# Performance work log

Measured on AMD Instinct MI355X. Metric: run time of the kernel, lower is better.

Reference implementation:

```python
import jax, jax.numpy as jnp
import numpy as np

N, E, D_LM, H, L, C = 100000, 1000000, 1024, 128, 3, 8


def setup_inputs() -> dict:
    key = jax.random.key(0)
    ks = jax.random.split(key, 8)
    return {
        "last_hidden_state": jax.random.normal(ks[0], (N, D_LM), jnp.float32),
        "edge_index": jax.random.randint(ks[1], (2, E), 0, N, dtype=jnp.int32),
        "W_lm": jax.random.normal(ks[2], (D_LM, H), jnp.float32) * 0.03,
        "b_lm": jnp.zeros((H,), jnp.float32),
        "W_gcn": jax.random.normal(ks[3], (L, H, H), jnp.float32) * 0.08,
        "b_gcn": jnp.zeros((L, H), jnp.float32),
        "W_cls": jax.random.normal(ks[4], (2 * H, C), jnp.float32) * 0.06,
        "b_cls": jnp.zeros((C,), jnp.float32),
    }


def reference(last_hidden_state, edge_index, W_lm, b_lm, W_gcn, b_gcn, W_cls, b_cls):
    # Frozen LM output -> lm_head (dropout is identity in eval mode)
    n = last_hidden_state.shape[0]
    lm = last_hidden_state @ W_lm + b_lm                      # [N, H]

    # GCN normalization (add self-loops, symmetric deg^{-1/2} norm), shared by all layers
    loops = jnp.arange(n, dtype=edge_index.dtype)
    src = jnp.concatenate([edge_index[0], loops])             # message sources j
    dst = jnp.concatenate([edge_index[1], loops])             # aggregation targets i
    deg = jax.ops.segment_sum(jnp.ones_like(dst, jnp.float32), dst, num_segments=n)
    dinv = jax.lax.rsqrt(jnp.maximum(deg, 1.0))               # deg >= 1 due to self-loops
    norm = dinv[src] * dinv[dst]                              # [E+N]

    out = lm
    for l in range(W_gcn.shape[0]):
        h = out @ W_gcn[l]                                    # linear transform first (PyG GCNConv)
        msg = h[src] * norm[:, None]                          # gather + scale  [E+N, H]
        out = jax.ops.segment_sum(msg, dst, num_segments=n) + b_gcn[l]
        out = jax.nn.relu(out)                                # dropout identity in eval

    logits = jnp.concatenate([lm, out], axis=-1) @ W_cls + b_cls  # [N, C]
    return logits
```

## Files before the change

### kernel.cpp

```cpp
#include <hip/hip_runtime.h>


using bf16x8 = __attribute__((ext_vector_type(8))) short;
using f32x4  = __attribute__((ext_vector_type(4))) float;
typedef unsigned short u16;
typedef unsigned int   u32;

__device__ __forceinline__ u16 f2bf(float f) {
  u32 u = __builtin_bit_cast(u32, f);
  u += 0x7fffu + ((u >> 16) & 1u);
  return (u16)(u >> 16);
}
__device__ __forceinline__ float bf2f(u32 lo16) {
  return __builtin_bit_cast(float, lo16 << 16);
}
__device__ __forceinline__ u32 packbf2(float a, float b) {
  u32 r;
  asm("v_cvt_pk_bf16_f32 %0, %1, %2" : "=v"(r) : "v"(a), "v"(b));
  return r;
}
__device__ __forceinline__ void gl_lds16(const void* g, void* l) {
  __builtin_amdgcn_global_load_lds(
      (const __attribute__((address_space(1))) void*)g,
      (__attribute__((address_space(3))) void*)l, 16, 0, 0);
}


__global__ void prep_fat(const float* __restrict__ Wlm, u16* __restrict__ WlmT,
                         const float* __restrict__ Wg, u16* __restrict__ WgT, int totalG) {
  int b = blockIdx.x;
  if (b < 512) {
    int idx = b * 256 + threadIdx.x;
    int k = idx >> 7, c = idx & 127;
    WlmT[c * 1024 + k] = f2bf(Wlm[idx]);
  } else {
    int idx = (b - 512) * 256 + threadIdx.x;
    if (idx < totalG) {
      int l = idx >> 14; int r = idx & 16383;
      int k = r >> 7, c = r & 127;
      WgT[l * 16384 + c * 128 + k] = f2bf(Wg[idx]);
    }
  }
}


__global__ void dinv_scanpart(const int* __restrict__ counts, float* __restrict__ dinv,
                              int* __restrict__ partials, int N) {
  __shared__ int sdata[256];
  int t = threadIdx.x;
  int base = blockIdx.x * 1024 + t * 4;
  int s = 0;
#pragma unroll
  for (int i = 0; i < 4; i++) {
    int idx = base + i;
    if (idx < N) {
      int c = counts[idx];
      s += c;
      dinv[idx] = rsqrtf((float)(c + 1));
    }
  }
  sdata[t] = s; __syncthreads();
  for (int off = 128; off > 0; off >>= 1) {
    if (t < off) sdata[t] += sdata[t + off];
    __syncthreads();
  }
  if (t == 0) partials[blockIdx.x] = sdata[0];
}


__global__ void scan_final2(const int* __restrict__ counts, const int* __restrict__ partials,
                            int* __restrict__ offsets, int N, int E, int NB) {
  __shared__ int sdata[256];
  int t = threadIdx.x;
  int pv = (t < NB && t < (int)blockIdx.x) ? partials[t] : 0;
  sdata[t] = pv; __syncthreads();
  for (int off = 128; off > 0; off >>= 1) {
    if (t < off) sdata[t] += sdata[t + off];
    __syncthreads();
  }
  int bse = sdata[0];
  __syncthreads();

  int bofs = blockIdx.x * 1024 + t * 4;
  int v[4]; int tsum = 0;
#pragma unroll
  for (int i = 0; i < 4; i++) { int idx = bofs + i; v[i] = (idx < N) ? counts[idx] : 0; tsum += v[i]; }
  sdata[t] = tsum; __syncthreads();
  int val = tsum;
  for (int off = 1; off < 256; off <<= 1) {
    int add = (t >= off) ? sdata[t - off] : 0;
    __syncthreads();
    val += add; sdata[t] = val;
    __syncthreads();
  }
  int run = bse + val - tsum;
#pragma unroll
  for (int i = 0; i < 4; i++) { int idx = bofs + i; if (idx < N) offsets[idx] = run; run += v[i]; }
  if (blockIdx.x == 0 && t == 0) offsets[N] = E;
}


__global__ __launch_bounds__(256) void gemm_lm_count_kernel(
    const float* __restrict__ A, const u16* __restrict__ Bt,
    const float* __restrict__ bias, u16* __restrict__ Out, int Nrows,
    const int* __restrict__ dst, int* __restrict__ counts, int E, int GB)
{
  __shared__ u16 lA[2][128 * 32];
  __shared__ u16 lB[2][128 * 32];
  if ((int)blockIdx.x >= GB) {
    int e = ((int)blockIdx.x - GB) * 256 + threadIdx.x;
    if (e < E) atomicAdd(&counts[dst[e]], 1);
    return;
  }
  const int t = threadIdx.x;
  const int lane = t & 63;
  const int w = t >> 6;
  const int wr = w >> 1, wc = w & 1;
  const long rowbase = (long)blockIdx.x * 128;
  const int quad = lane >> 4;
  const int l16 = lane & 15;

  const int seg0 = t, seg1 = t + 256;
  const int r0 = seg0 >> 2, kq0 = seg0 & 3;
  const int r1 = seg1 >> 2, kq1 = seg1 & 3;
  long g0 = rowbase + r0; if (g0 >= Nrows) g0 = Nrows - 1;
  long g1 = rowbase + r1; if (g1 >= Nrows) g1 = Nrows - 1;
  const float* Ab0 = A + g0 * 1024 + kq0 * 8;
  const float* Ab1 = A + g1 * 1024 + kq1 * 8;
  const int dA0 = (seg0 * 16) ^ ((r0 & 3) << 4);
  const int dA1 = (seg1 * 16) ^ ((r1 & 3) << 4);
  const char* Bsrc0 = (const char*)Bt + (size_t)r0 * 2048 + ((kq0 ^ (r0 & 3)) << 4);
  const char* Bsrc1 = (const char*)Bt + (size_t)r1 * 2048 + ((kq1 ^ (r1 & 3)) << 4);
  const int dB0 = seg0 * 16, dB1 = seg1 * 16;

  f32x4 acc[4][4];
#pragma unroll
  for (int i = 0; i < 4; i++)
#pragma unroll
    for (int j = 0; j < 4; j++) acc[i][j] = f32x4{0.f, 0.f, 0.f, 0.f};

  float4 fa[2][4];

#define GLB(KS, BUF) do { \
    gl_lds16(Bsrc0 + (size_t)(KS) * 64, (char*)lB[BUF] + dB0); \
    gl_lds16(Bsrc1 + (size_t)(KS) * 64, (char*)lB[BUF] + dB1); \
  } while (0)

#define ALOAD(KS, S) do { \
    fa[S][0] = *reinterpret_cast<const float4*>(Ab0 + (KS) * 32); \
    fa[S][1] = *reinterpret_cast<const float4*>(Ab0 + (KS) * 32 + 4); \
    fa[S][2] = *reinterpret_cast<const float4*>(Ab1 + (KS) * 32); \
    fa[S][3] = *reinterpret_cast<const float4*>(Ab1 + (KS) * 32 + 4); \
  } while (0)

#define APACK(S, BUF) do { \
    uint4 pk0, pk1; \
    pk0.x = packbf2(fa[S][0].x, fa[S][0].y); pk0.y = packbf2(fa[S][0].z, fa[S][0].w); \
    pk0.z = packbf2(fa[S][1].x, fa[S][1].y); pk0.w = packbf2(fa[S][1].z, fa[S][1].w); \
    pk1.x = packbf2(fa[S][2].x, fa[S][2].y); pk1.y = packbf2(fa[S][2].z, fa[S][2].w); \
    pk1.z = packbf2(fa[S][3].x, fa[S][3].y); pk1.w = packbf2(fa[S][3].z, fa[S][3].w); \
    *reinterpret_cast<uint4*>((char*)lA[BUF] + dA0) = pk0; \
    *reinterpret_cast<uint4*>((char*)lA[BUF] + dA1) = pk1; \
  } while (0)

#define FRAGS(BUF) do { \
    _Pragma("unroll") \
    for (int i = 0; i < 4; i++) { \
      int r = wr * 64 + i * 16 + l16; \
      af[i] = *reinterpret_cast<const bf16x8*>( \
          (const char*)lA[BUF] + r * 64 + ((quad ^ (r & 3)) << 4)); \
    } \
    _Pragma("unroll") \
    for (int j = 0; j < 4; j++) { \
      int c = wc * 64 + j * 16 + l16; \
      bfr[j] = *reinterpret_cast<const bf16x8*>( \
          (const char*)lB[BUF] + c * 64 + ((quad ^ (c & 3)) << 4)); \
    } \
  } while (0)

#define MFMA16() do { \
    _Pragma("unroll") \
    for (int i = 0; i < 4; i++) \
      _Pragma("unroll") \
      for (int j = 0; j < 4; j++) \
        acc[i][j] = __builtin_amdgcn_mfma_f32_16x16x32_bf16(af[i], bfr[j], acc[i][j], 0, 0, 0); \
  } while (0)

  GLB(0, 0);
  ALOAD(0, 0);
  ALOAD(1, 1);
  APACK(0, 0);
  asm volatile("s_waitcnt vmcnt(0) lgkmcnt(0)" ::: "memory");
  __builtin_amdgcn_s_barrier();
  __builtin_amdgcn_sched_barrier(0);

#define STEP_FULL(KS, BUF, SPACK, SLOAD) do { \
    bf16x8 af[4], bfr[4]; \
    FRAGS(BUF); \
    GLB((KS) + 1, BUF ^ 1); \
    APACK(SPACK, BUF ^ 1); \
    ALOAD((KS) + 2, SLOAD); \
    MFMA16(); \
    asm volatile("s_waitcnt vmcnt(4) lgkmcnt(0)" ::: "memory"); \
    __builtin_amdgcn_s_barrier(); \
    __builtin_amdgcn_sched_barrier(0); \
  } while (0)

  for (int ks = 0; ks < 30; ks += 2) {
    STEP_FULL(ks, 0, 1, 0);
    STEP_FULL(ks + 1, 1, 0, 1);
  }
  {
    bf16x8 af[4], bfr[4];
    FRAGS(0);
    GLB(31, 1);
    APACK(1, 1);
    MFMA16();
    asm volatile("s_waitcnt vmcnt(0) lgkmcnt(0)" ::: "memory");
    __builtin_amdgcn_s_barrier();
    __builtin_amdgcn_sched_barrier(0);
  }
  {
    bf16x8 af[4], bfr[4];
    FRAGS(1);
    MFMA16();
  }
#undef STEP_FULL
#undef MFMA16
#undef FRAGS
#undef APACK
#undef ALOAD
#undef GLB

#pragma unroll
  for (int i = 0; i < 4; i++) {
    long rbase = rowbase + wr * 64 + i * 16 + quad * 4;
#pragma unroll
    for (int j = 0; j < 4; j++) {
      int c = wc * 64 + j * 16 + l16;
      float bv = bias[c];
#pragma unroll
      for (int r = 0; r < 4; r++) {
        long grow = rbase + r;
        if (grow < Nrows)
          Out[(size_t)grow * 128 + c] = f2bf(acc[i][j][r] + bv);
      }
    }
  }
}


__device__ __forceinline__ void gemm128_body(
    u16* lA, u16* lB, int bid,
    const u16* __restrict__ A, const u16* __restrict__ Bt,
    const float* __restrict__ rs, u16* __restrict__ Out, int Nrows)
{
  const int t = threadIdx.x;
  const int lane = t & 63;
  const int w = t >> 6;
  const int wr = w >> 1, wc = w & 1;
  const int row0 = bid * 128;
  const int quad = lane >> 4;
  const int l16 = lane & 15;

#pragma unroll
  for (int rp = 0; rp < 8; rp++) {
    int o = (t + rp * 256) * 16;
    int row = o >> 8;
    int io = (o ^ ((row & 15) << 4)) & 255;
    long grow = (long)row0 + row;
    if (grow >= Nrows) grow = Nrows - 1;
    gl_lds16((const char*)A + grow * 256 + io, (char*)lA + o);
    gl_lds16((const char*)Bt + row * 256 + io, (char*)lB + o);
  }
  __syncthreads();

  f32x4 acc[4][4];
#pragma unroll
  for (int i = 0; i < 4; i++)
#pragma unroll
    for (int j = 0; j < 4; j++) acc[i][j] = f32x4{0.f, 0.f, 0.f, 0.f};

#pragma unroll
  for (int kk = 0; kk < 4; kk++) {
    bf16x8 af[4], bfr[4];
#pragma unroll
    for (int i = 0; i < 4; i++) {
      int r = wr * 64 + i * 16 + l16;
      int ch = (kk * 4 + quad) ^ (r & 15);
      af[i] = *reinterpret_cast<const bf16x8*>((const char*)lA + r * 256 + ch * 16);
    }
#pragma unroll
    for (int j = 0; j < 4; j++) {
      int c = wc * 64 + j * 16 + l16;
      int ch = (kk * 4 + quad) ^ (c & 15);
      bfr[j] = *reinterpret_cast<const bf16x8*>((const char*)lB + c * 256 + ch * 16);
    }
#pragma unroll
    for (int i = 0; i < 4; i++)
#pragma unroll
      for (int j = 0; j < 4; j++)
        acc[i][j] = __builtin_amdgcn_mfma_f32_16x16x32_bf16(af[i], bfr[j], acc[i][j], 0, 0, 0);
  }

#pragma unroll
  for (int i = 0; i < 4; i++) {
    int rbase = row0 + wr * 64 + i * 16 + quad * 4;
#pragma unroll
    for (int r = 0; r < 4; r++) {
      int grow = rbase + r;
      if (grow < Nrows) {
        float sc = rs[grow];
#pragma unroll
        for (int j = 0; j < 4; j++) {
          int c = wc * 64 + j * 16 + l16;
          Out[(size_t)grow * 128 + c] = f2bf(acc[i][j][r] * sc);
        }
      }
    }
  }
}

__global__ __launch_bounds__(256) void gemm128_kernel(
    const u16* __restrict__ A, const u16* __restrict__ Bt,
    const float* __restrict__ rs, u16* __restrict__ Out, int Nrows)
{
  __shared__ u16 lA[128 * 128];
  __shared__ u16 lB[128 * 128];
  gemm128_body(lA, lB, blockIdx.x, A, Bt, rs, Out, Nrows);
}

__global__ __launch_bounds__(256) void gemm128_fill_kernel(
    const u16* __restrict__ A, const u16* __restrict__ Bt,
    const float* __restrict__ rs, u16* __restrict__ Out, int Nrows,
    const int* __restrict__ src, const int* __restrict__ dst,
    const int* __restrict__ offsets, int* __restrict__ counts,
    int* __restrict__ col, int E, int GB)
{
  __shared__ u16 lA[128 * 128];
  __shared__ u16 lB[128 * 128];
  if ((int)blockIdx.x >= GB) {
    int e = ((int)blockIdx.x - GB) * 256 + threadIdx.x;
    if (e < E) {
      int d = dst[e];
      int p = offsets[d] + atomicSub(&counts[d], 1) - 1;
      col[p] = src[e];
    }
    return;
  }
  gemm128_body(lA, lB, blockIdx.x, A, Bt, rs, Out, Nrows);
}


#define BRED(v) do { v += __shfl_xor(v, 1);  v += __shfl_xor(v, 2);  v += __shfl_xor(v, 4); \
                     v += __shfl_xor(v, 8);  v += __shfl_xor(v, 16); v += __shfl_xor(v, 32); } while (0)

template<bool FINAL>
__global__ __launch_bounds__(256) void aggregate_kernel(
    const u16* __restrict__ h, const int* __restrict__ offsets,
    const int* __restrict__ col, const float* __restrict__ dinv,
    const float* __restrict__ bias, u16* __restrict__ outf,
    const u16* __restrict__ lm, const float* __restrict__ Wc,
    const float* __restrict__ bc, float* __restrict__ logits, int N)
{
  int w = threadIdx.x >> 6;
  int lane = threadIdx.x & 63;
  int i = blockIdx.x * 4 + w;
  if (i >= N) return;
  const u32* h32 = (const u32*)h;
  u32 us = h32[(size_t)i * 64 + lane];
  float ax = bf2f(us & 0xffffu), ay = bf2f(us >> 16);
  int s = offsets[i], e = offsets[i + 1];
  for (int base = s; base < e; base += 64) {
    int cnt = e - base; if (cnt > 64) cnt = 64;
    int cj = (base + lane < e) ? col[base + lane] : 0;
    int k = 0;
    for (; k + 4 <= cnt; k += 4) {
      int j0 = __shfl(cj, k),     j1 = __shfl(cj, k + 1);
      int j2 = __shfl(cj, k + 2), j3 = __shfl(cj, k + 3);
      u32 u0 = h32[(size_t)j0 * 64 + lane];
      u32 u1 = h32[(size_t)j1 * 64 + lane];
      u32 u2 = h32[(size_t)j2 * 64 + lane];
      u32 u3 = h32[(size_t)j3 * 64 + lane];
      ax += bf2f(u0 & 0xffffu); ay += bf2f(u0 >> 16);
      ax += bf2f(u1 & 0xffffu); ay += bf2f(u1 >> 16);
      ax += bf2f(u2 & 0xffffu); ay += bf2f(u2 >> 16);
      ax += bf2f(u3 & 0xffffu); ay += bf2f(u3 >> 16);
    }
    for (; k < cnt; k++) {
      int j = __shfl(cj, k);
      u32 uu = h32[(size_t)j * 64 + lane];
      ax += bf2f(uu & 0xffffu); ay += bf2f(uu >> 16);
    }
  }
  float di = dinv[i];
  ax = fmaxf(ax * di + bias[lane * 2], 0.f);
  ay = fmaxf(ay * di + bias[lane * 2 + 1], 0.f);
  if (!FINAL) {
    ((u32*)outf)[(size_t)i * 64 + lane] = packbf2(ax, ay);
  } else {
    u32 ul = ((const u32*)lm)[(size_t)i * 64 + lane];
    float lx = bf2f(ul & 0xffffu), ly = bf2f(ul >> 16);
    const float4* W4 = (const float4*)Wc;
    float4 a0 = W4[(2 * lane) * 2],       a1 = W4[(2 * lane) * 2 + 1];
    float4 b0 = W4[(2 * lane + 1) * 2],   b1 = W4[(2 * lane + 1) * 2 + 1];
    float4 c0 = W4[(128 + 2 * lane) * 2], c1 = W4[(128 + 2 * lane) * 2 + 1];
    float4 d0 = W4[(129 + 2 * lane) * 2], d1 = W4[(129 + 2 * lane) * 2 + 1];
    float s0 = lx * a0.x + ly * b0.x + ax * c0.x + ay * d0.x;
    float s1 = lx * a0.y + ly * b0.y + ax * c0.y + ay * d0.y;
    float s2 = lx * a0.z + ly * b0.z + ax * c0.z + ay * d0.z;
    float s3 = lx * a0.w + ly * b0.w + ax * c0.w + ay * d0.w;
    float s4 = lx * a1.x + ly * b1.x + ax * c1.x + ay * d1.x;
    float s5 = lx * a1.y + ly * b1.y + ax * c1.y + ay * d1.y;
    float s6 = lx * a1.z + ly * b1.z + ax * c1.z + ay * d1.z;
    float s7 = lx * a1.w + ly * b1.w + ax * c1.w + ay * d1.w;
    BRED(s0); BRED(s1); BRED(s2); BRED(s3); BRED(s4); BRED(s5); BRED(s6); BRED(s7);
    if (lane < 8) {
      float v = s0;
      v = (lane == 1) ? s1 : v;
      v = (lane == 2) ? s2 : v;
      v = (lane == 3) ? s3 : v;
      v = (lane == 4) ? s4 : v;
      v = (lane == 5) ? s5 : v;
      v = (lane == 6) ? s6 : v;
      v = (lane == 7) ? s7 : v;
      logits[(size_t)i * 8 + lane] = v + bc[lane];
    }
  }
}
#undef BRED


static inline char* bump(char*& p, size_t bytes) {
  char* r = p;
  p += (bytes + 255) & ~(size_t)255;
  return r;
}

extern "C" void kernel_launch(void* const* d_in, const int* in_sizes, int n_in,
                              void* d_out, int out_size, void* d_ws, size_t ws_size,
                              hipStream_t stream) {
  const float* X   = (const float*)d_in[0];
  const int*   EI  = (const int*)  d_in[1];
  const float* Wlm = (const float*)d_in[2];
  const float* blm = (const float*)d_in[3];
  const float* Wg  = (const float*)d_in[4];
  const float* bg  = (const float*)d_in[5];
  const float* Wc  = (const float*)d_in[6];
  const float* bc  = (const float*)d_in[7];
  float* out = (float*)d_out;

  const int N = in_sizes[0] / 1024;
  const int E = in_sizes[1] / 2;
  const int L = in_sizes[4] / (128 * 128);

  char* wp = (char*)d_ws;
  int*   counts  = (int*)  bump(wp, (size_t)N * 4);
  int*   offs    = (int*)  bump(wp, (size_t)(N + 1) * 4);
  float* dinv    = (float*)bump(wp, (size_t)N * 4);
  int*   partials= (int*)  bump(wp, 1024 * 4);
  int*   colA    = (int*)  bump(wp, (size_t)E * 4);
  u16*   WlmT    = (u16*)  bump(wp, (size_t)1024 * 128 * 2);
  u16*   WgT     = (u16*)  bump(wp, (size_t)L * 128 * 128 * 2);
  u16*   lmB     = (u16*)  bump(wp, (size_t)N * 128 * 2);
  u16*   hB      = (u16*)  bump(wp, (size_t)N * 128 * 2);
  u16*   featB   = (u16*)  bump(wp, (size_t)N * 128 * 2);

  hipMemsetAsync(counts, 0, (size_t)N * 4, stream);

  const int* srcp = EI;
  const int* dstp = EI + E;

  const int GB = (N + 127) / 128;
  const int CB = (E + 255) / 256;
  const int NB = (N + 1023) / 1024;
  const int PGB = (L * 128 * 128 + 255) / 256;

  prep_fat<<<512 + PGB, 256, 0, stream>>>(Wlm, WlmT, Wg, WgT, L * 128 * 128);
  gemm_lm_count_kernel<<<GB + CB, 256, 0, stream>>>(X, WlmT, blm, lmB, N, dstp, counts, E, GB);
  dinv_scanpart<<<NB, 256, 0, stream>>>(counts, dinv, partials, N);
  scan_final2<<<NB, 256, 0, stream>>>(counts, partials, offs, N, E, NB);
  gemm128_fill_kernel<<<GB + CB, 256, 0, stream>>>(lmB, WgT, dinv, hB, N,
                                                   srcp, dstp, offs, counts, colA, E, GB);

  const u16* cur;
  aggregate_kernel<false><<<(N + 3) / 4, 256, 0, stream>>>(
      hB, offs, colA, dinv, bg, featB, nullptr, nullptr, nullptr, nullptr, N);
  cur = featB;
  for (int l = 1; l < L; l++) {
    gemm128_kernel<<<GB, 256, 0, stream>>>(cur, WgT + (size_t)l * 16384, dinv, hB, N);
    if (l < L - 1) {
      aggregate_kernel<false><<<(N + 3) / 4, 256, 0, stream>>>(
          hB, offs, colA, dinv, bg + (size_t)l * 128, featB,
          nullptr, nullptr, nullptr, nullptr, N);
      cur = featB;
    } else {
      aggregate_kernel<true><<<(N + 3) / 4, 256, 0, stream>>>(
          hB, offs, colA, dinv, bg + (size_t)l * 128, nullptr,
          lmB, Wc, bc, out, N);
    }
  }
}
```

Measured before the change: 886.1 us.

## Fuse GCN aggregation with next-layer GEMM and merge scan kernels

Each intermediate GCN layer's aggregation now writes its 128-row tile into LDS and runs the next layer's 128x128 MFMA GEMM in the same block, so the bf16 feature buffer is no longer written to and re-read from global memory. The two-pass degree scan collapses into one kernel where each block recomputes its prefix by summing all earlier counts. The counts memset moves into the weight-prep kernel. In exchange, each 512-thread block runs 16 sequential gathers per wave before the GEMM, giving fewer blocks and less latency hiding on the gather. The redundant prefix sums also grow quadratically with the number of scan blocks.

```diff
diff --git a/kernel.cpp b/kernel.cpp
--- a/kernel.cpp
+++ b/kernel.cpp
@@ -27,64 +27,51 @@
 
 
 __global__ void prep_fat(const float* __restrict__ Wlm, u16* __restrict__ WlmT,
-                         const float* __restrict__ Wg, u16* __restrict__ WgT, int totalG) {
+                         const float* __restrict__ Wg, u16* __restrict__ WgT, int totalG,
+                         int* __restrict__ counts, int N, int PGB) {
   int b = blockIdx.x;
   if (b < 512) {
     int idx = b * 256 + threadIdx.x;
     int k = idx >> 7, c = idx & 127;
     WlmT[c * 1024 + k] = f2bf(Wlm[idx]);
-  } else {
+  } else if (b < 512 + PGB) {
     int idx = (b - 512) * 256 + threadIdx.x;
     if (idx < totalG) {
       int l = idx >> 14; int r = idx & 16383;
       int k = r >> 7, c = r & 127;
       WgT[l * 16384 + c * 128 + k] = f2bf(Wg[idx]);
     }
-  }
-}
-
-
-__global__ void dinv_scanpart(const int* __restrict__ counts, float* __restrict__ dinv,
-                              int* __restrict__ partials, int N) {
+  } else {
+    int idx = (b - 512 - PGB) * 256 + threadIdx.x;
+    if (idx < N) counts[idx] = 0;
+  }
+}
+
+
+__global__ void csr_scan(const int* __restrict__ counts, float* __restrict__ dinv,
+                         int* __restrict__ offsets, int N, int E) {
   __shared__ int sdata[256];
   int t = threadIdx.x;
-  int base = blockIdx.x * 1024 + t * 4;
-  int s = 0;
-#pragma unroll
-  for (int i = 0; i < 4; i++) {
-    int idx = base + i;
-    if (idx < N) {
-      int c = counts[idx];
-      s += c;
-      dinv[idx] = rsqrtf((float)(c + 1));
-    }
-  }
-  sdata[t] = s; __syncthreads();
+  int b = blockIdx.x;
+  int pre = 0;
+  for (int idx = t; idx < b * 1024; idx += 256) pre += counts[idx];
+  sdata[t] = pre; __syncthreads();
   for (int off = 128; off > 0; off >>= 1) {
     if (t < off) sdata[t] += sdata[t + off];
     __syncthreads();
   }
-  if (t == 0) partials[blockIdx.x] = sdata[0];
-}
-
-
-__global__ void scan_final2(const int* __restrict__ counts, const int* __restrict__ partials,
-                            int* __restrict__ offsets, int N, int E, int NB) {
-  __shared__ int sdata[256];
-  int t = threadIdx.x;
-  int pv = (t < NB && t < (int)blockIdx.x) ? partials[t] : 0;
-  sdata[t] = pv; __syncthreads();
-  for (int off = 128; off > 0; off >>= 1) {
-    if (t < off) sdata[t] += sdata[t + off];
-    __syncthreads();
-  }
   int bse = sdata[0];
   __syncthreads();
 
-  int bofs = blockIdx.x * 1024 + t * 4;
+  int bofs = b * 1024 + t * 4;
   int v[4]; int tsum = 0;
 #pragma unroll
-  for (int i = 0; i < 4; i++) { int idx = bofs + i; v[i] = (idx < N) ? counts[idx] : 0; tsum += v[i]; }
+  for (int i = 0; i < 4; i++) {
+    int idx = bofs + i;
+    int c = (idx < N) ? counts[idx] : 0;
+    v[i] = c; tsum += c;
+    if (idx < N) dinv[idx] = rsqrtf((float)(c + 1));
+  }
   sdata[t] = tsum; __syncthreads();
   int val = tsum;
   for (int off = 1; off < 256; off <<= 1) {
@@ -96,7 +83,7 @@
   int run = bse + val - tsum;
 #pragma unroll
   for (int i = 0; i < 4; i++) { int idx = bofs + i; if (idx < N) offsets[idx] = run; run += v[i]; }
-  if (blockIdx.x == 0 && t == 0) offsets[N] = E;
+  if (b == 0 && t == 0) offsets[N] = E;
 }
 
 
@@ -319,15 +306,6 @@
       }
     }
   }
-}
-
-__global__ __launch_bounds__(256) void gemm128_kernel(
-    const u16* __restrict__ A, const u16* __restrict__ Bt,
-    const float* __restrict__ rs, u16* __restrict__ Out, int Nrows)
-{
-  __shared__ u16 lA[128 * 128];
-  __shared__ u16 lB[128 * 128];
-  gemm128_body(lA, lB, blockIdx.x, A, Bt, rs, Out, Nrows);
 }
 
 __global__ __launch_bounds__(256) void gemm128_fill_kernel(
@@ -352,14 +330,126 @@
 }
 
 
+__global__ __launch_bounds__(512) void agg_gemm_kernel(
+    const u16* __restrict__ h, const int* __restrict__ offsets,
+    const int* __restrict__ col, const float* __restrict__ dinv,
+    const float* __restrict__ bias, const u16* __restrict__ Bt,
+    u16* __restrict__ Out, int Nrows)
+{
+  __shared__ u16 lA[128 * 128];
+  __shared__ u16 lB[128 * 128];
+  const int t = threadIdx.x;
+  const int lane = t & 63;
+  const int w = t >> 6;
+  const int row0 = blockIdx.x * 128;
+
+#pragma unroll
+  for (int rp = 0; rp < 4; rp++) {
+    int o = (t + rp * 512) * 16;
+    int row = o >> 8;
+    int io = (o ^ ((row & 15) << 4)) & 255;
+    gl_lds16((const char*)Bt + row * 256 + io, (char*)lB + o);
+  }
+
+  const u32* h32 = (const u32*)h;
+  const float bx = bias[lane * 2];
+  const float by = bias[lane * 2 + 1];
+  for (int rr = 0; rr < 16; rr++) {
+    int r = w * 16 + rr;
+    int i = row0 + r;
+    u32 wv = 0;
+    if (i < Nrows) {
+      u32 us = h32[(size_t)i * 64 + lane];
+      float ax = bf2f(us & 0xffffu), ay = bf2f(us >> 16);
+      int s = offsets[i], e = offsets[i + 1];
+      for (int base = s; base < e; base += 64) {
+        int cnt = e - base; if (cnt > 64) cnt = 64;
+        int cj = (base + lane < e) ? col[base + lane] : 0;
+        int k = 0;
+        for (; k + 4 <= cnt; k += 4) {
+          int j0 = __shfl(cj, k),     j1 = __shfl(cj, k + 1);
+          int j2 = __shfl(cj, k + 2), j3 = __shfl(cj, k + 3);
+          u32 u0 = h32[(size_t)j0 * 64 + lane];
+          u32 u1 = h32[(size_t)j1 * 64 + lane];
+          u32 u2 = h32[(size_t)j2 * 64 + lane];
+          u32 u3 = h32[(size_t)j3 * 64 + lane];
+          ax += bf2f(u0 & 0xffffu); ay += bf2f(u0 >> 16);
+          ax += bf2f(u1 & 0xffffu); ay += bf2f(u1 >> 16);
+          ax += bf2f(u2 & 0xffffu); ay += bf2f(u2 >> 16);
+          ax += bf2f(u3 & 0xffffu); ay += bf2f(u3 >> 16);
+        }
+        for (; k < cnt; k++) {
+          int j = __shfl(cj, k);
+          u32 uu = h32[(size_t)j * 64 + lane];
+          ax += bf2f(uu & 0xffffu); ay += bf2f(uu >> 16);
+        }
+      }
+      float di = dinv[i];
+      ax = fmaxf(ax * di + bx, 0.f);
+      ay = fmaxf(ay * di + by, 0.f);
+      wv = packbf2(ax, ay);
+    }
+    *reinterpret_cast<u32*>((char*)lA + r * 256 +
+        ((((lane >> 2) ^ (r & 15)) << 4) + ((lane & 3) << 2))) = wv;
+  }
+  __syncthreads();
+
+  const int wr = w >> 2, wc = w & 3;
+  const int quad = lane >> 4, l16 = lane & 15;
+  f32x4 acc[4][2];
+#pragma unroll
+  for (int i = 0; i < 4; i++)
+#pragma unroll
+    for (int j = 0; j < 2; j++) acc[i][j] = f32x4{0.f, 0.f, 0.f, 0.f};
+
+#pragma unroll
+  for (int kk = 0; kk < 4; kk++) {
+    bf16x8 af[4], bfr[2];
+#pragma unroll
+    for (int i = 0; i < 4; i++) {
+      int r = wr * 64 + i * 16 + l16;
+      int ch = (kk * 4 + quad) ^ (r & 15);
+      af[i] = *reinterpret_cast<const bf16x8*>((const char*)lA + r * 256 + ch * 16);
+    }
+#pragma unroll
+    for (int j = 0; j < 2; j++) {
+      int c = wc * 32 + j * 16 + l16;
+      int ch = (kk * 4 + quad) ^ (c & 15);
+      bfr[j] = *reinterpret_cast<const bf16x8*>((const char*)lB + c * 256 + ch * 16);
+    }
+#pragma unroll
+    for (int i = 0; i < 4; i++)
+#pragma unroll
+      for (int j = 0; j < 2; j++)
+        acc[i][j] = __builtin_amdgcn_mfma_f32_16x16x32_bf16(af[i], bfr[j], acc[i][j], 0, 0, 0);
+  }
+
+#pragma unroll
+  for (int i = 0; i < 4; i++) {
+    int rbase = row0 + wr * 64 + i * 16 + quad * 4;
+#pragma unroll
+    for (int r = 0; r < 4; r++) {
+      int grow = rbase + r;
+      if (grow < Nrows) {
+        float sc = dinv[grow];
+#pragma unroll
+        for (int j = 0; j < 2; j++) {
+          int c = wc * 32 + j * 16 + l16;
+          Out[(size_t)grow * 128 + c] = f2bf(acc[i][j][r] * sc);
+        }
+      }
+    }
+  }
+}
+
+
 #define BRED(v) do { v += __shfl_xor(v, 1);  v += __shfl_xor(v, 2);  v += __shfl_xor(v, 4); \
                      v += __shfl_xor(v, 8);  v += __shfl_xor(v, 16); v += __shfl_xor(v, 32); } while (0)
 
-template<bool FINAL>
-__global__ __launch_bounds__(256) void aggregate_kernel(
+__global__ __launch_bounds__(256) void aggregate_final_kernel(
     const u16* __restrict__ h, const int* __restrict__ offsets,
     const int* __restrict__ col, const float* __restrict__ dinv,
-    const float* __restrict__ bias, u16* __restrict__ outf,
+    const float* __restrict__ bias,
     const u16* __restrict__ lm, const float* __restrict__ Wc,
     const float* __restrict__ bc, float* __restrict__ logits, int N)
 {
@@ -396,36 +486,33 @@
   float di = dinv[i];
   ax = fmaxf(ax * di + bias[lane * 2], 0.f);
   ay = fmaxf(ay * di + bias[lane * 2 + 1], 0.f);
-  if (!FINAL) {
-    ((u32*)outf)[(size_t)i * 64 + lane] = packbf2(ax, ay);
-  } else {
-    u32 ul = ((const u32*)lm)[(size_t)i * 64 + lane];
-    float lx = bf2f(ul & 0xffffu), ly = bf2f(ul >> 16);
-    const float4* W4 = (const float4*)Wc;
-    float4 a0 = W4[(2 * lane) * 2],       a1 = W4[(2 * lane) * 2 + 1];
-    float4 b0 = W4[(2 * lane + 1) * 2],   b1 = W4[(2 * lane + 1) * 2 + 1];
-    float4 c0 = W4[(128 + 2 * lane) * 2], c1 = W4[(128 + 2 * lane) * 2 + 1];
-    float4 d0 = W4[(129 + 2 * lane) * 2], d1 = W4[(129 + 2 * lane) * 2 + 1];
-    float s0 = lx * a0.x + ly * b0.x + ax * c0.x + ay * d0.x;
-    float s1 = lx * a0.y + ly * b0.y + ax * c0.y + ay * d0.y;
-    float s2 = lx * a0.z + ly * b0.z + ax * c0.z + ay * d0.z;
-    float s3 = lx * a0.w + ly * b0.w + ax * c0.w + ay * d0.w;
-    float s4 = lx * a1.x + ly * b1.x + ax * c1.x + ay * d1.x;
-    float s5 = lx * a1.y + ly * b1.y + ax * c1.y + ay * d1.y;
-    float s6 = lx * a1.z + ly * b1.z + ax * c1.z + ay * d1.z;
-    float s7 = lx * a1.w + ly * b1.w + ax * c1.w + ay * d1.w;
-    BRED(s0); BRED(s1); BRED(s2); BRED(s3); BRED(s4); BRED(s5); BRED(s6); BRED(s7);
-    if (lane < 8) {
-      float v = s0;
-      v = (lane == 1) ? s1 : v;
-      v = (lane == 2) ? s2 : v;
-      v = (lane == 3) ? s3 : v;
-      v = (lane == 4) ? s4 : v;
-      v = (lane == 5) ? s5 : v;
-      v = (lane == 6) ? s6 : v;
-      v = (lane == 7) ? s7 : v;
-      logits[(size_t)i * 8 + lane] = v + bc[lane];
-    }
+
+  u32 ul = ((const u32*)lm)[(size_t)i * 64 + lane];
+  float lx = bf2f(ul & 0xffffu), ly = bf2f(ul >> 16);
+  const float4* W4 = (const float4*)Wc;
+  float4 a0 = W4[(2 * lane) * 2],       a1 = W4[(2 * lane) * 2 + 1];
+  float4 b0 = W4[(2 * lane + 1) * 2],   b1 = W4[(2 * lane + 1) * 2 + 1];
+  float4 c0 = W4[(128 + 2 * lane) * 2], c1 = W4[(128 + 2 * lane) * 2 + 1];
+  float4 d0 = W4[(129 + 2 * lane) * 2], d1 = W4[(129 + 2 * lane) * 2 + 1];
+  float s0 = lx * a0.x + ly * b0.x + ax * c0.x + ay * d0.x;
+  float s1 = lx * a0.y + ly * b0.y + ax * c0.y + ay * d0.y;
+  float s2 = lx * a0.z + ly * b0.z + ax * c0.z + ay * d0.z;
+  float s3 = lx * a0.w + ly * b0.w + ax * c0.w + ay * d0.w;
+  float s4 = lx * a1.x + ly * b1.x + ax * c1.x + ay * d1.x;
+  float s5 = lx * a1.y + ly * b1.y + ax * c1.y + ay * d1.y;
+  float s6 = lx * a1.z + ly * b1.z + ax * c1.z + ay * d1.z;
+  float s7 = lx * a1.w + ly * b1.w + ax * c1.w + ay * d1.w;
+  BRED(s0); BRED(s1); BRED(s2); BRED(s3); BRED(s4); BRED(s5); BRED(s6); BRED(s7);
+  if (lane < 8) {
+    float v = s0;
+    v = (lane == 1) ? s1 : v;
+    v = (lane == 2) ? s2 : v;
+    v = (lane == 3) ? s3 : v;
+    v = (lane == 4) ? s4 : v;
+    v = (lane == 5) ? s5 : v;
+    v = (lane == 6) ? s6 : v;
+    v = (lane == 7) ? s7 : v;
+    logits[(size_t)i * 8 + lane] = v + bc[lane];
   }
 }
 #undef BRED
@@ -458,46 +545,30 @@
   int*   counts  = (int*)  bump(wp, (size_t)N * 4);
   int*   offs    = (int*)  bump(wp, (size_t)(N + 1) * 4);
   float* dinv    = (float*)bump(wp, (size_t)N * 4);
-  int*   partials= (int*)  bump(wp, 1024 * 4);
   int*   colA    = (int*)  bump(wp, (size_t)E * 4);
   u16*   WlmT    = (u16*)  bump(wp, (size_t)1024 * 128 * 2);
   u16*   WgT     = (u16*)  bump(wp, (size_t)L * 128 * 128 * 2);
   u16*   lmB     = (u16*)  bump(wp, (size_t)N * 128 * 2);
   u16*   hB      = (u16*)  bump(wp, (size_t)N * 128 * 2);
-  u16*   featB   = (u16*)  bump(wp, (size_t)N * 128 * 2);
-
-  hipMemsetAsync(counts, 0, (size_t)N * 4, stream);
+  u16*   hB2     = (u16*)  bump(wp, (size_t)N * 128 * 2);
 
   const int* srcp = EI;
   const int* dstp = EI + E;
 
-  const int GB = (N + 127) / 128;
-  const int CB = (E + 255) / 256;
-  const int NB = (N + 1023) / 1024;
+  const int GB  = (N + 127) / 128;
+  const int CB  = (E + 255) / 256;
+  const int NB  = (N + 1023) / 1024;
   const int PGB = (L * 128 * 128 + 255) / 256;
-
-  prep_fat<<<512 + PGB, 256, 0, stream>>>(Wlm, WlmT, Wg, WgT, L * 128 * 128);
+  const int ZB  = (N + 255) / 256;
+
+  prep_fat<<<512 + PGB + ZB, 256, 0, stream>>>(Wlm, WlmT, Wg, WgT, L * 128 * 128,
+                                               counts, N, PGB);
   gemm_lm_count_kernel<<<GB + CB, 256, 0, stream>>>(X, WlmT, blm, lmB, N, dstp, counts, E, GB);
-  dinv_scanpart<<<NB, 256, 0, stream>>>(counts, dinv, partials, N);
-  scan_final2<<<NB, 256, 0, stream>>>(counts, partials, offs, N, E, NB);
+  csr_scan<<<NB, 256, 0, stream>>>(counts, dinv, offs, N, E);
   gemm128_fill_kernel<<<GB + CB, 256, 0, stream>>>(lmB, WgT, dinv, hB, N,
                                                    srcp, dstp, offs, counts, colA, E, GB);
-
-  const u16* cur;
-  aggregate_kernel<false><<<(N + 3) / 4, 256, 0, stream>>>(
-      hB, offs, colA, dinv, bg, featB, nullptr, nullptr, nullptr, nullptr, N);
-  cur = featB;
-  for (int l = 1; l < L; l++) {
-    gemm128_kernel<<<GB, 256, 0, stream>>>(cur, WgT + (size_t)l * 16384, dinv, hB, N);
-    if (l < L - 1) {
-      aggregate_kernel<false><<<(N + 3) / 4, 256, 0, stream>>>(
-          hB, offs, colA, dinv, bg + (size_t)l * 128, featB,
-          nullptr, nullptr, nullptr, nullptr, N);
-      cur = featB;
-    } else {
-      aggregate_kernel<true><<<(N + 3) / 4, 256, 0, stream>>>(
-          hB, offs, colA, dinv, bg + (size_t)l * 128, nullptr,
-          lmB, Wc, bc, out, N);
-    }
-  }
-}
+  agg_gemm_kernel<<<GB, 512, 0, stream>>>(hB, offs, colA, dinv, bg, WgT + 16384, hB2, N);
+  agg_gemm_kernel<<<GB, 512, 0, stream>>>(hB2, offs, colA, dinv, bg + 128, WgT + 2 * 16384, hB, N);
+  aggregate_final_kernel<<<(N + 3) / 4, 256, 0, stream>>>(
+      hB, offs, colA, dinv, bg + 2 * 128, lmB, Wc, bc, out, N);
+}
```

Result: slower. 987.1 us (+11.4%).
